# Kernel tuning notes

Measured on AMD Instinct MI355X. Metric: run time of the kernel, lower is better.

The kernel has to match this reference:

```python
import jax, jax.numpy as jnp
import numpy as np

B, C, T, H, W, TS = 4, 512, 2048, 8, 16, 1000
D = C // H  # head_dim = 64
SCALE = D ** -0.5


def _conv1x1(w, b, z):
    # torch Conv1d(dim, dim, 1): (B,C,T) -> (B,C,T)
    return jnp.einsum('oc,bct->bot', w, z) + b[None, :, None]


def _linear(w, b, z):
    # torch Linear: z @ w.T + b, w is (out,in)
    return z @ w.T + b


def _rope(x, cos, sin):
    # x: (B,H,T,D); cos/sin: (T, D//2) broadcast over (B,H)
    x1, x2 = x[..., ::2], x[..., 1::2]
    r = jnp.stack([x1 * cos - x2 * sin, x1 * sin + x2 * cos], axis=-1)
    return r.reshape(x.shape)


def _local(x, cond, qw, qb, kw, kb, vw, vb, ow, ob):
    q = _conv1x1(qw, qb, x)
    k = _conv1x1(kw, kb, cond)
    v = _conv1x1(vw, vb, cond)
    pl = W // 2
    pr = W - pl - 1
    kp = jnp.pad(k, ((0, 0), (0, 0), (pl, pr)))
    vp = jnp.pad(v, ((0, 0), (0, 0), (pl, pr)))
    idx = jnp.arange(T)[:, None] + jnp.arange(W)[None, :]  # (T,W)
    ku = kp[:, :, idx].reshape(B, H, D, T, W)
    vu = vp[:, :, idx].reshape(B, H, D, T, W)
    qh = q.reshape(B, H, D, T)
    dots = jnp.einsum('bhdt,bhdtw->bhtw', qh, ku) * SCALE
    attn = jax.nn.softmax(dots, axis=-1)
    out = jnp.einsum('bhtw,bhdtw->bhdt', attn, vu)
    # faithful to torch: permute(0,1,3,2).contiguous().view(B,C,T)
    out = out.transpose(0, 1, 3, 2).reshape(B, C, T)
    return _conv1x1(ow, ob, out)


def _global(xg, cg, qw, qb, kw, kb, vw, vb, ow, ob):
    # xg, cg: (B,T,C)
    q = _linear(qw, qb, xg).reshape(B, T, H, D).transpose(0, 2, 1, 3)
    k = _linear(kw, kb, cg).reshape(B, T, H, D).transpose(0, 2, 1, 3)
    v = _linear(vw, vb, cg).reshape(B, T, H, D).transpose(0, 2, 1, 3)
    inv_freq = 1.0 / (10000.0 ** (jnp.arange(0, D, 2, dtype=jnp.float32) / D))
    pos = jnp.arange(T, dtype=jnp.float32)
    sinus = pos[:, None] * inv_freq[None, :]  # (T, D//2)
    cos, sin = jnp.cos(sinus), jnp.sin(sinus)
    q = _rope(q, cos, sin)
    k = _rope(k, cos, sin)
    dots = jnp.einsum('bhqd,bhkd->bhqk', q, k) * SCALE
    attn = jax.nn.softmax(dots, axis=-1)
    out = jnp.einsum('bhqk,bhkd->bhqd', attn, v)
    out = out.transpose(0, 2, 1, 3).reshape(B, T, C)
    return _linear(ow, ob, out)


def setup_inputs() -> dict:
    key = jax.random.key(0)
    ks = jax.random.split(key, 20)
    pm = lambda k: jax.random.normal(k, (C, C), dtype=jnp.float32) * 0.02
    pb = lambda k: jax.random.normal(k, (C,), dtype=jnp.float32) * 0.02
    return {
        'x': jax.random.normal(ks[0], (B, C, T), dtype=jnp.float32),
        'cond': jax.random.normal(ks[1], (B, C, T), dtype=jnp.float32),
        't': jax.random.randint(ks[2], (B,), 0, TS),
        'lq_w': pm(ks[3]), 'lq_b': pb(ks[4]),
        'lk_w': pm(ks[5]), 'lk_b': pb(ks[6]),
        'lv_w': pm(ks[7]), 'lv_b': pb(ks[8]),
        'lo_w': pm(ks[9]), 'lo_b': pb(ks[10]),
        'gq_w': pm(ks[11]), 'gq_b': pb(ks[12]),
        'gk_w': pm(ks[13]), 'gk_b': pb(ks[14]),
        'gv_w': pm(ks[15]), 'gv_b': pb(ks[16]),
        'go_w': pm(ks[17]), 'go_b': pb(ks[18]),
    }


def reference(x, cond, t, lq_w, lq_b, lk_w, lk_b, lv_w, lv_b, lo_w, lo_b,
              gq_w, gq_b, gk_w, gk_b, gv_w, gv_b, go_w, go_b):
    ctx_local = _local(x, cond, lq_w, lq_b, lk_w, lk_b, lv_w, lv_b, lo_w, lo_b)
    ctx_global = _global(x.transpose(0, 2, 1), cond.transpose(0, 2, 1),
                         gq_w, gq_b, gk_w, gk_b, gv_w, gv_b, go_w, go_b)
    ctx_global = ctx_global.transpose(0, 2, 1)  # (B,C,T)
    t_norm = t.astype(jnp.float32) / jnp.float32(TS - 1)
    a_g = (1.0 - t_norm)[:, None, None]
    a_l = t_norm[:, None, None]
    return jnp.sqrt(a_g) * ctx_global + jnp.sqrt(a_l) * ctx_local
```

## Files before the change

### kernel.cpp

```cpp
#include <hip/hip_runtime.h>
#include <math.h>

#define BB 4
#define CC 512
#define TT 2048
#define HH 8
#define DD 64

static constexpr float SCALE = 0.125f;
static constexpr float QK_SCALE_LOG2 = 0.125f * 1.4426950408889634f;

typedef __attribute__((ext_vector_type(8)))  short  short8;
typedef __attribute__((ext_vector_type(4)))  float  f32x4;
typedef __attribute__((ext_vector_type(16))) float  f32x16;
typedef __attribute__((ext_vector_type(2)))  unsigned int u32x2;

static __device__ __forceinline__ ushort f2bf(float f) {
    uint u = __float_as_uint(f);
    uint r = (u + 0x7fffu + ((u >> 16) & 1u)) >> 16;
    return (ushort)r;
}
static __device__ __forceinline__ float bf2f(ushort u) {
    return __uint_as_float((uint)u << 16);
}

typedef unsigned int u32;
typedef u32 __attribute__((address_space(1))) gu32;
typedef u32 __attribute__((address_space(3))) lu32;
static __device__ __forceinline__ void gload_lds16(const void* g, void* l) {
    __builtin_amdgcn_global_load_lds((const gu32*)g, (lu32*)l, 16, 0, 0);
}

__global__ __launch_bounds__(256)
void prep_kernel(const float* __restrict__ x, const float* __restrict__ cond,
                 const float* w0, const float* w1, const float* w2, const float* w3,
                 const float* w4, const float* w5, const float* w6, const float* w7,
                 ushort* __restrict__ wbf, ushort* __restrict__ wc,
                 ushort* __restrict__ xtb, ushort* __restrict__ ctb,
                 float* __restrict__ ctab, float* __restrict__ stab)
{
    __shared__ ushort L[64][66];
    int bid = blockIdx.x;
    const int tid = threadIdx.x;

    if (bid < 256) {
        int idx = bid * 256 + tid;
        int i = idx >> 11;
        int t = idx & 2047;
        float ex   = (2.0f * (float)i) / 64.0f;
        float invf = powf(10000.0f, -ex);
        float ang  = (float)t * invf;
        ctab[idx] = cosf(ang);
        stab[idx] = sinf(ang);
        return;
    }
    bid -= 256;
    if (bid < 2048) {
        const float* srcs[8] = {w0, w1, w2, w3, w4, w5, w6, w7};
        int wi = bid >> 8;
        int idx = ((bid & 255) * 256 + tid) * 4;
        float4 v = *(const float4*)&srcs[wi][idx];
        uint lo = (uint)f2bf(v.x) | ((uint)f2bf(v.y) << 16);
        uint hi = (uint)f2bf(v.z) | ((uint)f2bf(v.w) << 16);
        uint2 pk = make_uint2(lo, hi);
        if (wi < 6) {
            *(uint2*)&wbf[(size_t)wi * 262144 + idx] = pk;
        } else {
            int row = idx >> 9, col = idx & 511;
            *(uint2*)&wc[(size_t)row * 1024 + (wi - 6) * 512 + col] = pk;
        }
        return;
    }
    bid -= 2048;
    const int z = bid >> 8;
    const int r = bid & 255;
    const float* in = (z < 4) ? x : cond;
    ushort* outp    = (z < 4) ? xtb : ctb;
    const int b = z & 3;
    const int t0 = (r & 31) * 64, c0 = (r >> 5) * 64;
    const float* inb = in + (size_t)b * CC * TT;
    ushort* outb = outp + (size_t)b * TT * CC;
    const int lc = tid >> 6;
    const int lt = tid & 63;
    #pragma unroll
    for (int i = 0; i < 16; i++) {
        int c = i * 4 + lc;
        L[c][lt] = f2bf(inb[(size_t)(c0 + c) * TT + t0 + lt]);
    }
    __syncthreads();
    #pragma unroll
    for (int i = 0; i < 16; i++) {
        int t = i * 4 + lc;
        outb[(size_t)(t0 + t) * CC + c0 + lt] = L[lt][t];
    }
}

__global__ __launch_bounds__(256)
void transpose_bf16_kernel(const ushort* __restrict__ in, ushort* __restrict__ AG)
{
    __shared__ ushort L[64][66];
    const int t0 = blockIdx.x * 64, c0 = blockIdx.y * 64, b = blockIdx.z;
    const ushort* inb = in + (size_t)b * CC * TT;
    ushort* outb = AG + (size_t)b * TT * 1024;
    const int lc = threadIdx.x >> 6;
    const int lt = threadIdx.x & 63;
    #pragma unroll
    for (int i = 0; i < 16; i++) {
        int c = i * 4 + lc;
        L[c][lt] = inb[(size_t)(c0 + c) * TT + t0 + lt];
    }
    __syncthreads();
    #pragma unroll
    for (int i = 0; i < 16; i++) {
        int t = i * 4 + lc;
        outb[(size_t)(t0 + t) * 1024 + c0 + lt] = L[lt][t];
    }
}

#define GEMM_BODY(Wp, XTp, KD, NB)                                                  \
    __shared__ __align__(16) ushort As[2][128][32];                                 \
    __shared__ __align__(16) ushort Bs[2][NB][32];                                  \
    const int tid  = threadIdx.x;                                                   \
    const int wid  = tid >> 6;                                                      \
    const int lane = tid & 63;                                                      \
    const int x  = lane & 15;                                                       \
    const int gq = lane >> 4;                                                       \
    const int wm = wid >> 1, wn = wid & 1;                                          \
    const int m0 = blockIdx.y * 128;                                                \
    const int n0 = blockIdx.x * NB;                                                 \
    const int srow = lane >> 2;                                                     \
    const int sblk = lane & 3;                                                      \
    f32x4 acc[4][NB / 32];                                                          \
    _Pragma("unroll")                                                               \
    for (int i = 0; i < 4; i++)                                                     \
        _Pragma("unroll")                                                           \
        for (int j = 0; j < NB / 32; j++) acc[i][j] = (f32x4){0.f, 0.f, 0.f, 0.f};  \
    auto stage = [&](int bf, int k0) {                                              \
        _Pragma("unroll")                                                           \
        for (int c = 0; c < 2; c++) {                                               \
            int row = c * 64 + wid * 16 + srow;                                     \
            int dbk = sblk ^ ((row >> 1) & 3);                                      \
            gload_lds16(&Wp[(size_t)(m0 + row) * KD + k0 + dbk * 8],                \
                        &As[bf][c * 64 + wid * 16][0]);                             \
            if (c * 64 < NB)                                                        \
                gload_lds16(&XTp[(size_t)(n0 + row) * KD + k0 + dbk * 8],           \
                            &Bs[bf][c * 64 + wid * 16][0]);                         \
        }                                                                           \
    };                                                                              \
    stage(0, 0);                                                                    \
    __syncthreads();                                                                \
    for (int ks = 0; ks < (KD) / 32; ks++) {                                        \
        int cur = ks & 1;                                                           \
        if (ks < (KD) / 32 - 1) stage(cur ^ 1, (ks + 1) * 32);                      \
        short8 aF[4], bF[NB / 32];                                                  \
        _Pragma("unroll")                                                           \
        for (int mi = 0; mi < 4; mi++) {                                            \
            int row = wm * 64 + mi * 16 + x;                                        \
            aF[mi] = *(const short8*)&As[cur][row][(gq ^ ((row >> 1) & 3)) * 8];    \
        }                                                                           \
        _Pragma("unroll")                                                           \
        for (int nj = 0; nj < NB / 32; nj++) {                                      \
            int row = wn * (NB / 2) + nj * 16 + x;                                  \
            bF[nj] = *(const short8*)&Bs[cur][row][(gq ^ ((row >> 1) & 3)) * 8];    \
        }                                                                           \
        _Pragma("unroll")                                                           \
        for (int mi = 0; mi < 4; mi++)                                              \
            _Pragma("unroll")                                                       \
            for (int nj = 0; nj < NB / 32; nj++)                                    \
                acc[mi][nj] = __builtin_amdgcn_mfma_f32_16x16x32_bf16(aF[mi], bF[nj], acc[mi][nj], 0, 0, 0); \
        __syncthreads();                                                            \
    }

__global__ __launch_bounds__(256)
void gemm6_kernel(const ushort* __restrict__ wbase,
                  const float* __restrict__ b0, const float* __restrict__ b1, const float* __restrict__ b2,
                  const float* __restrict__ b3, const float* __restrict__ b4, const float* __restrict__ b5,
                  const ushort* __restrict__ xtb, const ushort* __restrict__ ctb,
                  ushort* __restrict__ y0, ushort* __restrict__ y1, ushort* __restrict__ y2,
                  ushort* __restrict__ y3, ushort* __restrict__ y4, ushort* __restrict__ y5,
                  const float* __restrict__ ctab, const float* __restrict__ stab)
{
    const int z = blockIdx.z;
    const ushort* Wp  = wbase + (size_t)z * 262144;
    const float* bias = (z == 0) ? b0 : (z == 1) ? b1 : (z == 2) ? b2 : (z == 3) ? b3 : (z == 4) ? b4 : b5;
    const ushort* XTp = (z == 0 || z == 3) ? xtb : ctb;
    ushort* Y = (z == 0) ? y0 : (z == 1) ? y1 : (z == 2) ? y2 : (z == 3) ? y3 : (z == 4) ? y4 : y5;
    const bool do_rope = (z == 3 || z == 4);
    const float qscale = (z == 3) ? QK_SCALE_LOG2 : 1.0f;

    GEMM_BODY(Wp, XTp, 512, 128)

    const int bidx = (n0 + wn * 64) >> 11;
    #pragma unroll
    for (int mi = 0; mi < 4; mi++) {
        const int mb = m0 + wm * 64 + mi * 16 + 4 * gq;
        float bv[4];
        #pragma unroll
        for (int r = 0; r < 4; r++) bv[r] = bias[mb + r];
        #pragma unroll
        for (int nj = 0; nj < 4; nj++) {
            const int n  = n0 + wn * 64 + nj * 16 + x;
            const int tt = n & 2047;
            f32x4 v = acc[mi][nj];
            v[0] += bv[0]; v[1] += bv[1]; v[2] += bv[2]; v[3] += bv[3];
            if (do_rope) {
                const int i0 = (mb & 63) >> 1;
                float c0 = ctab[(size_t)i0 * 2048 + tt],       s0 = stab[(size_t)i0 * 2048 + tt];
                float c1 = ctab[(size_t)(i0 + 1) * 2048 + tt], s1 = stab[(size_t)(i0 + 1) * 2048 + tt];
                float e0 = (v[0] * c0 - v[1] * s0) * qscale;
                float e1 = (v[0] * s0 + v[1] * c0) * qscale;
                float e2 = (v[2] * c1 - v[3] * s1) * qscale;
                float e3 = (v[2] * s1 + v[3] * c1) * qscale;
                v[0] = e0; v[1] = e1; v[2] = e2; v[3] = e3;
            }
            if (z != 5) {
                uint lo = (uint)f2bf(v[0]) | ((uint)f2bf(v[1]) << 16);
                uint hi = (uint)f2bf(v[2]) | ((uint)f2bf(v[3]) << 16);
                *(uint2*)&Y[(size_t)n * 512 + mb] = make_uint2(lo, hi);
            } else {
                #pragma unroll
                for (int r = 0; r < 4; r++)
                    Y[((size_t)bidx * 512 + mb + r) * 2048 + tt] = f2bf(v[r]);
            }
        }
    }
}

__global__ __launch_bounds__(256)
void gemm_comb_kernel(const ushort* __restrict__ Wp,
                      const float* __restrict__ bl, const float* __restrict__ bg,
                      const ushort* __restrict__ XTp, float* __restrict__ Y,
                      const int* __restrict__ tarr)
{
    GEMM_BODY(Wp, XTp, 1024, 64)

    const int bidx = (n0 + wn * 32) >> 11;
    float tn = (float)tarr[bidx] / 999.0f;
    float sl = sqrtf(tn), sg = sqrtf(1.0f - tn);

    #pragma unroll
    for (int mi = 0; mi < 4; mi++) {
        const int mb = m0 + wm * 64 + mi * 16 + 4 * gq;
        float bv[4];
        #pragma unroll
        for (int r = 0; r < 4; r++) bv[r] = sl * bl[mb + r] + sg * bg[mb + r];
        #pragma unroll
        for (int nj = 0; nj < 2; nj++) {
            const int tt = (n0 + wn * 32 + nj * 16 + x) & 2047;
            f32x4 v = acc[mi][nj];
            #pragma unroll
            for (int r = 0; r < 4; r++)
                Y[((size_t)bidx * 512 + mb + r) * 2048 + tt] = v[r] + bv[r];
        }
    }
}

__global__ __launch_bounds__(256)
void local_attn_kernel(const ushort* __restrict__ qt, const ushort* __restrict__ kt,
                       const ushort* __restrict__ vt, ushort* __restrict__ outb,
                       const int* __restrict__ tarr)
{
    int gidx = blockIdx.x * 256 + threadIdx.x;
    int t  = gidx & (TT - 1);
    int bh = gidx >> 11;
    int h  = bh & (HH - 1);
    int b  = bh >> 3;
    const size_t rb = (size_t)b * TT;
    const int co = h * DD;
    const float wl = sqrtf((float)tarr[b] / 999.0f);

    float qf[64];
    {
        const ushort* qp = qt + (rb + t) * 512 + co;
        #pragma unroll
        for (int i = 0; i < 8; i++) {
            short8 v = *(const short8*)&qp[i * 8];
            #pragma unroll
            for (int j = 0; j < 8; j++) qf[i * 8 + j] = bf2f((ushort)v[j]);
        }
    }

    int koff[16]; float msk[16];
    #pragma unroll
    for (int w = 0; w < 16; w++) {
        int kidx = t + w - 8;
        msk[w]  = (kidx >= 0 && kidx < TT) ? 1.0f : 0.0f;
        koff[w] = min(max(kidx, 0), TT - 1);
    }

    float dots[16];
    #pragma unroll
    for (int w = 0; w < 16; w++) {
        const ushort* kp = kt + (rb + koff[w]) * 512 + co;
        float d0 = 0.f, d1 = 0.f;
        #pragma unroll
        for (int i = 0; i < 8; i++) {
            short8 v = *(const short8*)&kp[i * 8];
            #pragma unroll
            for (int j = 0; j < 8; j += 2) {
                d0 = fmaf(qf[i * 8 + j],     bf2f((ushort)v[j]),     d0);
                d1 = fmaf(qf[i * 8 + j + 1], bf2f((ushort)v[j + 1]), d1);
            }
        }
        dots[w] = d0 + d1;
    }

    float m = -1e30f;
    #pragma unroll
    for (int w = 0; w < 16; w++) { dots[w] = dots[w] * SCALE * msk[w]; m = fmaxf(m, dots[w]); }
    float p[16], s = 0.f;
    #pragma unroll
    for (int w = 0; w < 16; w++) { p[w] = __expf(dots[w] - m); s += p[w]; }
    float inv = wl / s;
    #pragma unroll
    for (int w = 0; w < 16; w++) p[w] *= msk[w] * inv;

    float oa[64];
    #pragma unroll
    for (int d = 0; d < 64; d++) oa[d] = 0.f;
    #pragma unroll
    for (int w = 0; w < 16; w++) {
        const ushort* vp = vt + (rb + koff[w]) * 512 + co;
        #pragma unroll
        for (int i = 0; i < 8; i++) {
            short8 v = *(const short8*)&vp[i * 8];
            #pragma unroll
            for (int j = 0; j < 8; j++)
                oa[i * 8 + j] = fmaf(p[w], bf2f((ushort)v[j]), oa[i * 8 + j]);
        }
    }

    ushort* op = outb + ((size_t)b * CC + co + (t >> 5)) * TT + (size_t)(t & 31) * DD;
    #pragma unroll
    for (int i = 0; i < 16; i++) {
        uint lo = (uint)f2bf(oa[i * 4 + 0]) | ((uint)f2bf(oa[i * 4 + 1]) << 16);
        uint hi = (uint)f2bf(oa[i * 4 + 2]) | ((uint)f2bf(oa[i * 4 + 3]) << 16);
        *(uint2*)&op[i * 4] = make_uint2(lo, hi);
    }
}

__global__ __launch_bounds__(128)
void flash_global_kernel(const ushort* __restrict__ qtd, const ushort* __restrict__ ktd,
                         const ushort* __restrict__ vb, ushort* __restrict__ AG,
                         const int* __restrict__ tarr)
{
    __shared__ __align__(16) ushort Ks[2][4096];
    __shared__ __align__(16) ushort Vs[2][4096];

    const int tid  = threadIdx.x;
    const int w    = tid >> 6;
    const int lane = tid & 63;
    const int qh   = lane & 31;
    const int h    = lane >> 5;

    const int bid = blockIdx.x;
    const int sw  = (bid & 7) * 128 + (bid >> 3);
    const int q0  = (sw & 31) * 64;
    const int p   = sw >> 5;
    const int hh  = p & 7;
    const int b   = p >> 3;

    const size_t bh_ct = ((size_t)b * CC + hh * DD) * TT;
    const size_t btd   = (size_t)b * TT;
    const int q_glob = q0 + w * 32 + qh;
    const float sg_mix = sqrtf(1.0f - (float)tarr[b] / 999.0f);

    short8 aQ[4];
    {
        const ushort* qrow = qtd + (btd + q_glob) * 512 + hh * 64;
        #pragma unroll
        for (int kap = 0; kap < 4; kap++)
            aQ[kap] = *(const short8*)&qrow[kap * 16 + h * 8];
    }

    f32x16 oacc[2];
    #pragma unroll
    for (int d = 0; d < 2; d++)
        #pragma unroll
        for (int r = 0; r < 16; r++) oacc[d][r] = 0.f;
    float l_run = 0.0f;

    const int srow = tid >> 3;
    const int spos = tid & 7;
    const int sblk2 = spos ^ (srow & 7);
    const ushort* kptr = ktd + (btd + srow) * 512 + hh * 64 + sblk2 * 8;
    const ushort* vptr = vb + bh_ct + (size_t)srow * TT + sblk2 * 8;

    auto issue = [&](int buf) {
        #pragma unroll
        for (int j = 0; j < 4; j++)
            gload_lds16(kptr + (size_t)j * 16 * 512, &Ks[buf][w * 512 + j * 1024]);
        #pragma unroll
        for (int j = 0; j < 4; j++)
            gload_lds16(vptr + (size_t)j * 16 * TT, &Vs[buf][w * 512 + j * 1024]);
        kptr += 64 * 512; vptr += 64;
    };
    issue(0);

    int cur = 0;
    for (int kt = 0; kt < 32; kt++) {
        __syncthreads();
        if (kt < 31) issue(cur ^ 1);

        const ushort* KsC = &Ks[cur][0];
        const ushort* VsC = &Vs[cur][0];

        f32x16 ST[2];
        #pragma unroll
        for (int sb = 0; sb < 2; sb++)
            #pragma unroll
            for (int r = 0; r < 16; r++) ST[sb][r] = 0.f;
        __builtin_amdgcn_s_setprio(1);
        #pragma unroll
        for (int sb = 0; sb < 2; sb++) {
            const int row = sb * 32 + qh;
            #pragma unroll
            for (int kap = 0; kap < 4; kap++) {
                short8 aK = *(const short8*)&KsC[row * 64 + (((kap * 2 + h) ^ (row & 7)) << 3)];
                ST[sb] = __builtin_amdgcn_mfma_f32_32x32x16_bf16(aK, aQ[kap], ST[sb], 0, 0, 0);
            }
        }
        __builtin_amdgcn_s_setprio(0);

        float s0 = 0.f, s1 = 0.f, s2 = 0.f, s3 = 0.f;
        #pragma unroll
        for (int sb = 0; sb < 2; sb++)
            #pragma unroll
            for (int r = 0; r < 16; r += 4) {
                ST[sb][r + 0] = __builtin_amdgcn_exp2f(ST[sb][r + 0]);
                ST[sb][r + 1] = __builtin_amdgcn_exp2f(ST[sb][r + 1]);
                ST[sb][r + 2] = __builtin_amdgcn_exp2f(ST[sb][r + 2]);
                ST[sb][r + 3] = __builtin_amdgcn_exp2f(ST[sb][r + 3]);
                s0 += ST[sb][r + 0]; s1 += ST[sb][r + 1];
                s2 += ST[sb][r + 2]; s3 += ST[sb][r + 3];
            }
        l_run += (s0 + s1) + (s2 + s3);

        short8 bP[4];
        #pragma unroll
        for (int sb = 0; sb < 2; sb++)
            #pragma unroll
            for (int kcp = 0; kcp < 2; kcp++) {
                const int rb2 = kcp * 8;
                uint ca, cb, cc, cd;
                asm("v_cvt_pk_bf16_f32 %0, %1, %2" : "=v"(ca) : "v"(ST[sb][rb2 + 0]), "v"(ST[sb][rb2 + 1]));
                asm("v_cvt_pk_bf16_f32 %0, %1, %2" : "=v"(cb) : "v"(ST[sb][rb2 + 2]), "v"(ST[sb][rb2 + 3]));
                asm("v_cvt_pk_bf16_f32 %0, %1, %2" : "=v"(cc) : "v"(ST[sb][rb2 + 4]), "v"(ST[sb][rb2 + 5]));
                asm("v_cvt_pk_bf16_f32 %0, %1, %2" : "=v"(cd) : "v"(ST[sb][rb2 + 6]), "v"(ST[sb][rb2 + 7]));
                u32x2 r1 = __builtin_amdgcn_permlane32_swap(ca, cc, false, false);
                u32x2 r2 = __builtin_amdgcn_permlane32_swap(cb, cd, false, false);
                uint4 bu = make_uint4(r1[0], r2[0], r1[1], r2[1]);
                bP[sb * 2 + kcp] = __builtin_bit_cast(short8, bu);
            }

        __builtin_amdgcn_s_setprio(1);
        #pragma unroll
        for (int db = 0; db < 2; db++) {
            const int row = db * 32 + qh;
            #pragma unroll
            for (int kc = 0; kc < 4; kc++) {
                short8 aV = *(const short8*)&VsC[row * 64 + (((kc * 2 + h) ^ (row & 7)) << 3)];
                oacc[db] = __builtin_amdgcn_mfma_f32_32x32x16_bf16(aV, bP[kc], oacc[db], 0, 0, 0);
            }
        }
        __builtin_amdgcn_s_setprio(0);
        cur ^= 1;
    }

    float ltot = l_run + __shfl_xor(l_run, 32);
    float inv = sg_mix / ltot;
    ushort* agrow = AG + (btd + q_glob) * 1024 + 512 + hh * 64;
    #pragma unroll
    for (int db = 0; db < 2; db++)
        #pragma unroll
        for (int rq = 0; rq < 4; rq++) {
            const int d0 = db * 32 + rq * 8 + h * 4;
            uint lo = (uint)f2bf(oacc[db][rq * 4 + 0] * inv) | ((uint)f2bf(oacc[db][rq * 4 + 1] * inv) << 16);
            uint hi = (uint)f2bf(oacc[db][rq * 4 + 2] * inv) | ((uint)f2bf(oacc[db][rq * 4 + 3] * inv) << 16);
            *(uint2*)&agrow[d0] = make_uint2(lo, hi);
        }
}

extern "C" void kernel_launch(void* const* d_in, const int* in_sizes, int n_in,
                              void* d_out, int out_size, void* d_ws, size_t ws_size,
                              hipStream_t stream)
{
    const float* x    = (const float*)d_in[0];
    const float* cond = (const float*)d_in[1];
    const int*   tarr = (const int*)d_in[2];
    const float* lq_w = (const float*)d_in[3];
    const float* lq_b = (const float*)d_in[4];
    const float* lk_w = (const float*)d_in[5];
    const float* lk_b = (const float*)d_in[6];
    const float* lv_w = (const float*)d_in[7];
    const float* lv_b = (const float*)d_in[8];
    const float* lo_w = (const float*)d_in[9];
    const float* lo_b = (const float*)d_in[10];
    const float* gq_w = (const float*)d_in[11];
    const float* gq_b = (const float*)d_in[12];
    const float* gk_w = (const float*)d_in[13];
    const float* gk_b = (const float*)d_in[14];
    const float* gv_w = (const float*)d_in[15];
    const float* gv_b = (const float*)d_in[16];
    const float* go_w = (const float*)d_in[17];
    const float* go_b = (const float*)d_in[18];
    float* out = (float*)d_out;

    const size_t N = (size_t)BB * CC * TT;
    char* w = (char*)d_ws;
    ushort* xtb = (ushort*)w; w += N * 2;
    ushort* ctb = (ushort*)w; w += N * 2;
    ushort* lq  = (ushort*)w; w += N * 2;
    ushort* lk  = (ushort*)w; w += N * 2;
    ushort* lv  = (ushort*)w; w += N * 2;
    ushort* gqb = (ushort*)w; w += N * 2;
    ushort* gkb = (ushort*)w; w += N * 2;
    ushort* gvb = (ushort*)w; w += N * 2;
    ushort* scr = (ushort*)w; w += N * 2;
    ushort* AG  = (ushort*)w; w += (size_t)BB * TT * 1024 * 2;
    ushort* wbf = (ushort*)w; w += (size_t)6 * 512 * 512 * 2;
    ushort* wc  = (ushort*)w; w += (size_t)512 * 1024 * 2;
    float* ctab = (float*)w;  w += (size_t)32 * 2048 * 4;
    float* stab = (float*)w;

    dim3 blk(256);

    prep_kernel<<<dim3(4352), blk, 0, stream>>>(x, cond,
                                                lq_w, lk_w, lv_w, gq_w, gk_w, gv_w, lo_w, go_w,
                                                wbf, wc, xtb, ctb, ctab, stab);

    gemm6_kernel<<<dim3(64, 4, 6), blk, 0, stream>>>(wbf, lq_b, lk_b, lv_b, gq_b, gk_b, gv_b,
                                                     xtb, ctb, lq, lk, lv, gqb, gkb, gvb, ctab, stab);

    local_attn_kernel<<<dim3(BB * HH * TT / 256), blk, 0, stream>>>(lq, lk, lv, scr, tarr);
    transpose_bf16_kernel<<<dim3(32, 8, BB), blk, 0, stream>>>(scr, AG);

    flash_global_kernel<<<dim3(1024), dim3(128), 0, stream>>>(gqb, gkb, gvb, AG, tarr);

    gemm_comb_kernel<<<dim3(128, 4), blk, 0, stream>>>(wc, lo_b, go_b, AG, out, tarr);
}
```

Baseline: 181.9 us.

## Pre-swizzle K/V into MFMA fragment layout and load directly to registers

The projection GEMM now writes global K and V in a layout that matches the MFMA operand fragments. The flash attention kernel can then read each fragment with one coalesced 16-byte load per lane straight into registers, with no LDS staging and no __syncthreads. The flash kernel drops to one wave per block with twice as many blocks, and prefetches the next K/V tile into registers while computing. In exchange, each wave re-reads K/V from global/L2 with no cross-wave sharing through LDS, and the register prefetch raises register pressure. The V store in the GEMM epilogue also becomes a scattered 2-byte write pattern.

```diff
diff --git a/kernel.cpp b/kernel.cpp
--- a/kernel.cpp
+++ b/kernel.cpp
@@ -213,14 +213,30 @@
                 float e3 = (v[2] * s1 + v[3] * c1) * qscale;
                 v[0] = e0; v[1] = e1; v[2] = e2; v[3] = e3;
             }
-            if (z != 5) {
+            if (z <= 3) {
                 uint lo = (uint)f2bf(v[0]) | ((uint)f2bf(v[1]) << 16);
                 uint hi = (uint)f2bf(v[2]) | ((uint)f2bf(v[3]) << 16);
                 *(uint2*)&Y[(size_t)n * 512 + mb] = make_uint2(lo, hi);
+            } else if (z == 4) {
+                const int hh = (mb >> 6) & 7;
+                const int d  = mb & 63;
+                const int kap = d >> 4, hb = (d >> 3) & 1, j0 = d & 7;
+                const int kt = tt >> 6, tk = tt & 63, sb = tk >> 5, qh = tk & 31;
+                size_t off = ((size_t)(bidx * 8 + hh)) * 131072
+                           + (size_t)(((((kt * 2 + sb) * 4 + kap) * 2 + hb) * 32 + qh) * 8 + j0);
+                uint lo = (uint)f2bf(v[0]) | ((uint)f2bf(v[1]) << 16);
+                uint hi = (uint)f2bf(v[2]) | ((uint)f2bf(v[3]) << 16);
+                *(uint2*)&Y[off] = make_uint2(lo, hi);
             } else {
+                const int hh = (mb >> 6) & 7;
+                const int qh0 = mb & 31, db = (mb & 63) >> 5;
+                const int kt = tt >> 6, kk = tt & 63;
+                const int kc = kk >> 4, hb = (kk >> 3) & 1, j = kk & 7;
+                size_t base = ((size_t)(bidx * 8 + hh)) * 131072
+                            + (size_t)(((((kt * 2 + db) * 4 + kc) * 2 + hb) * 32 + qh0) * 8 + j);
                 #pragma unroll
                 for (int r = 0; r < 4; r++)
-                    Y[((size_t)bidx * 512 + mb + r) * 2048 + tt] = f2bf(v[r]);
+                    Y[base + (size_t)r * 8] = f2bf(v[r]);
             }
         }
     }
@@ -339,34 +355,31 @@
     }
 }
 
-__global__ __launch_bounds__(128)
-void flash_global_kernel(const ushort* __restrict__ qtd, const ushort* __restrict__ ktd,
-                         const ushort* __restrict__ vb, ushort* __restrict__ AG,
+__global__ __launch_bounds__(64)
+void flash_global_kernel(const ushort* __restrict__ qtd, const ushort* __restrict__ KT,
+                         const ushort* __restrict__ VT, ushort* __restrict__ AG,
                          const int* __restrict__ tarr)
 {
-    __shared__ __align__(16) ushort Ks[2][4096];
-    __shared__ __align__(16) ushort Vs[2][4096];
-
-    const int tid  = threadIdx.x;
-    const int w    = tid >> 6;
-    const int lane = tid & 63;
-    const int qh   = lane & 31;
-    const int h    = lane >> 5;
+    const int lane = threadIdx.x;
+    const int qh = lane & 31;
 
     const int bid = blockIdx.x;
-    const int sw  = (bid & 7) * 128 + (bid >> 3);
-    const int q0  = (sw & 31) * 64;
-    const int p   = sw >> 5;
-    const int hh  = p & 7;
-    const int b   = p >> 3;
-
-    const size_t bh_ct = ((size_t)b * CC + hh * DD) * TT;
-    const size_t btd   = (size_t)b * TT;
-    const int q_glob = q0 + w * 32 + qh;
+    const int sw  = (bid & 7) * 256 + (bid >> 3);
+    const int qt  = sw & 63;
+    const int p   = sw >> 6;
+    const int hh  = p & 7, b = p >> 3;
+
+    const size_t kvbase = (size_t)p * 131072;
+    const size_t btd    = (size_t)b * TT;
+    const int q_glob = qt * 32 + qh;
     const float sg_mix = sqrtf(1.0f - (float)tarr[b] / 999.0f);
+
+    const ushort* Kb = KT + kvbase;
+    const ushort* Vb = VT + kvbase;
 
     short8 aQ[4];
     {
+        const int h = lane >> 5;
         const ushort* qrow = qtd + (btd + q_glob) * 512 + hh * 64;
         #pragma unroll
         for (int kap = 0; kap < 4; kap++)
@@ -380,31 +393,21 @@
         for (int r = 0; r < 16; r++) oacc[d][r] = 0.f;
     float l_run = 0.0f;
 
-    const int srow = tid >> 3;
-    const int spos = tid & 7;
-    const int sblk2 = spos ^ (srow & 7);
-    const ushort* kptr = ktd + (btd + srow) * 512 + hh * 64 + sblk2 * 8;
-    const ushort* vptr = vb + bh_ct + (size_t)srow * TT + sblk2 * 8;
-
-    auto issue = [&](int buf) {
-        #pragma unroll
-        for (int j = 0; j < 4; j++)
-            gload_lds16(kptr + (size_t)j * 16 * 512, &Ks[buf][w * 512 + j * 1024]);
-        #pragma unroll
-        for (int j = 0; j < 4; j++)
-            gload_lds16(vptr + (size_t)j * 16 * TT, &Vs[buf][w * 512 + j * 1024]);
-        kptr += 64 * 512; vptr += 64;
+    short8 kf[8], vf[8];
+    auto loadK = [&](int kt) {
+        #pragma unroll
+        for (int i = 0; i < 8; i++)
+            kf[i] = *(const short8*)&Kb[(size_t)(kt * 8 + i) * 512 + lane * 8];
     };
-    issue(0);
-
-    int cur = 0;
+    auto loadV = [&](int kt) {
+        #pragma unroll
+        for (int i = 0; i < 8; i++)
+            vf[i] = *(const short8*)&Vb[(size_t)(kt * 8 + i) * 512 + lane * 8];
+    };
+    loadK(0);
+    loadV(0);
+
     for (int kt = 0; kt < 32; kt++) {
-        __syncthreads();
-        if (kt < 31) issue(cur ^ 1);
-
-        const ushort* KsC = &Ks[cur][0];
-        const ushort* VsC = &Vs[cur][0];
-
         f32x16 ST[2];
         #pragma unroll
         for (int sb = 0; sb < 2; sb++)
@@ -412,15 +415,13 @@
             for (int r = 0; r < 16; r++) ST[sb][r] = 0.f;
         __builtin_amdgcn_s_setprio(1);
         #pragma unroll
-        for (int sb = 0; sb < 2; sb++) {
-            const int row = sb * 32 + qh;
-            #pragma unroll
-            for (int kap = 0; kap < 4; kap++) {
-                short8 aK = *(const short8*)&KsC[row * 64 + (((kap * 2 + h) ^ (row & 7)) << 3)];
-                ST[sb] = __builtin_amdgcn_mfma_f32_32x32x16_bf16(aK, aQ[kap], ST[sb], 0, 0, 0);
-            }
-        }
+        for (int sb = 0; sb < 2; sb++)
+            #pragma unroll
+            for (int kap = 0; kap < 4; kap++)
+                ST[sb] = __builtin_amdgcn_mfma_f32_32x32x16_bf16(kf[sb * 4 + kap], aQ[kap], ST[sb], 0, 0, 0);
         __builtin_amdgcn_s_setprio(0);
+
+        if (kt < 31) loadK(kt + 1);
 
         float s0 = 0.f, s1 = 0.f, s2 = 0.f, s3 = 0.f;
         #pragma unroll
@@ -455,18 +456,16 @@
 
         __builtin_amdgcn_s_setprio(1);
         #pragma unroll
-        for (int db = 0; db < 2; db++) {
-            const int row = db * 32 + qh;
-            #pragma unroll
-            for (int kc = 0; kc < 4; kc++) {
-                short8 aV = *(const short8*)&VsC[row * 64 + (((kc * 2 + h) ^ (row & 7)) << 3)];
-                oacc[db] = __builtin_amdgcn_mfma_f32_32x32x16_bf16(aV, bP[kc], oacc[db], 0, 0, 0);
-            }
-        }
+        for (int db = 0; db < 2; db++)
+            #pragma unroll
+            for (int kc = 0; kc < 4; kc++)
+                oacc[db] = __builtin_amdgcn_mfma_f32_32x32x16_bf16(vf[db * 4 + kc], bP[kc], oacc[db], 0, 0, 0);
         __builtin_amdgcn_s_setprio(0);
-        cur ^= 1;
-    }
-
+
+        if (kt < 31) loadV(kt + 1);
+    }
+
+    const int h = lane >> 5;
     float ltot = l_run + __shfl_xor(l_run, 32);
     float inv = sg_mix / ltot;
     ushort* agrow = AG + (btd + q_glob) * 1024 + 512 + hh * 64;
@@ -514,8 +513,8 @@
     ushort* lk  = (ushort*)w; w += N * 2;
     ushort* lv  = (ushort*)w; w += N * 2;
     ushort* gqb = (ushort*)w; w += N * 2;
-    ushort* gkb = (ushort*)w; w += N * 2;
-    ushort* gvb = (ushort*)w; w += N * 2;
+    ushort* ktb = (ushort*)w; w += N * 2;
+    ushort* vtb = (ushort*)w; w += N * 2;
     ushort* scr = (ushort*)w; w += N * 2;
     ushort* AG  = (ushort*)w; w += (size_t)BB * TT * 1024 * 2;
     ushort* wbf = (ushort*)w; w += (size_t)6 * 512 * 512 * 2;
@@ -530,12 +529,12 @@
                                                 wbf, wc, xtb, ctb, ctab, stab);
 
     gemm6_kernel<<<dim3(64, 4, 6), blk, 0, stream>>>(wbf, lq_b, lk_b, lv_b, gq_b, gk_b, gv_b,
-                                                     xtb, ctb, lq, lk, lv, gqb, gkb, gvb, ctab, stab);
+                                                     xtb, ctb, lq, lk, lv, gqb, ktb, vtb, ctab, stab);
 
     local_attn_kernel<<<dim3(BB * HH * TT / 256), blk, 0, stream>>>(lq, lk, lv, scr, tarr);
     transpose_bf16_kernel<<<dim3(32, 8, BB), blk, 0, stream>>>(scr, AG);
 
-    flash_global_kernel<<<dim3(1024), dim3(128), 0, stream>>>(gqb, gkb, gvb, AG, tarr);
+    flash_global_kernel<<<dim3(2048), dim3(64), 0, stream>>>(gqb, ktb, vtb, AG, tarr);
 
     gemm_comb_kernel<<<dim3(128, 4), blk, 0, stream>>>(wc, lo_b, go_b, AG, out, tarr);
 }
```

Measured after the change: 177.7 us. 2.3% less time.
